# Optimization experiments

Measured on AMD Instinct MI355X. Metric: run time of the kernel, lower is better.

Reference implementation:

```python
import jax, jax.numpy as jnp
import numpy as np
from functools import partial

B, T, IN, H, NC, L = 2048, 512, 64, 64, 4, 2


def _lstm_layer(x, w_ih, w_hh, b_ih, b_hh):
    """Single PyTorch-convention LSTM layer. x: [B,T,Din]; gates ordered i,f,g,o.
    Returns full hidden sequence [B,T,H]."""
    Bx = x.shape[0]
    Hh = w_hh.shape[1]
    # precompute input contribution for all timesteps: [T,B,4H]
    xg = jnp.einsum('bti,gi->tbg', x, w_ih) + (b_ih + b_hh)

    def step(carry, xg_t):
        h, c = carry
        gates = xg_t + h @ w_hh.T  # [B,4H]
        i, f, g, o = jnp.split(gates, 4, axis=-1)
        i = jax.nn.sigmoid(i)
        f = jax.nn.sigmoid(f)
        g = jnp.tanh(g)
        o = jax.nn.sigmoid(o)
        c = f * c + i * g
        h = o * jnp.tanh(c)
        return (h, c), h

    h0 = jnp.zeros((Bx, Hh), dtype=x.dtype)
    c0 = jnp.zeros((Bx, Hh), dtype=x.dtype)
    (_, _), hs = jax.lax.scan(step, (h0, c0), xg)  # hs: [T,B,H]
    return jnp.swapaxes(hs, 0, 1)  # [B,T,H]


def setup_inputs() -> dict:
    key = jax.random.key(0)
    ks = jax.random.split(key, 16)
    s_in = 1.0 / np.sqrt(H)
    inp = {"x": jax.random.normal(ks[0], (B, T, IN), dtype=jnp.float32)}
    dims = [IN, H]
    for l in range(L):
        inp[f"w_ih{l}"] = jax.random.uniform(ks[1 + 4 * l], (4 * H, dims[l]), jnp.float32, -s_in, s_in)
        inp[f"w_hh{l}"] = jax.random.uniform(ks[2 + 4 * l], (4 * H, H), jnp.float32, -s_in, s_in)
        inp[f"b_ih{l}"] = jax.random.uniform(ks[3 + 4 * l], (4 * H,), jnp.float32, -s_in, s_in)
        inp[f"b_hh{l}"] = jax.random.uniform(ks[4 + 4 * l], (4 * H,), jnp.float32, -s_in, s_in)
    inp["fc_w"] = jax.random.uniform(ks[9], (NC, H), jnp.float32, -s_in, s_in)
    inp["fc_b"] = jax.random.uniform(ks[10], (NC,), jnp.float32, -s_in, s_in)
    return inp


def reference(x, w_ih0, w_hh0, b_ih0, b_hh0, w_ih1, w_hh1, b_ih1, b_hh1, fc_w, fc_b):
    # layer 0
    h1 = _lstm_layer(x, w_ih0, w_hh0, b_ih0, b_hh0)   # [B,T,H]
    # inter-layer dropout: identity at inference
    h2 = _lstm_layer(h1, w_ih1, w_hh1, b_ih1, b_hh1)  # [B,T,H]
    last = h2[:, -1, :]                                # [B,H]; dropout = identity (eval)
    return last @ fc_w.T + fc_b                        # [B,NC]
```

## Files before the change

### kernel.cpp

```cpp
#include <hip/hip_runtime.h>
#include <stdint.h>


#define T_SEQ 512
#define NB    4
#define PSTR  136

typedef __attribute__((ext_vector_type(8))) short  short8;
typedef __attribute__((ext_vector_type(4))) float  float4v;

__device__ __forceinline__ unsigned short f2bf(float f) {
    unsigned int u = __builtin_bit_cast(unsigned int, f);
    return (unsigned short)((u + 0x7FFFu + ((u >> 16) & 1u)) >> 16);
}
__device__ __forceinline__ float bf2f(unsigned short h) {
    unsigned int u = ((unsigned int)h) << 16;
    return __builtin_bit_cast(float, u);
}
__device__ __forceinline__ float sigm(float x) {
    return __builtin_amdgcn_rcpf(1.0f + __builtin_amdgcn_exp2f(-1.44269504088896f * x));
}
__device__ __forceinline__ float tanh_f(float x) {
    float a = __builtin_fabsf(x);
    float e = __builtin_amdgcn_exp2f(-2.88539008177793f * a);
    float t = (1.0f - e) * __builtin_amdgcn_rcpf(1.0f + e);
    return __builtin_copysignf(t, x);
}
__device__ __forceinline__ float permx32(float v) {
    int p = __builtin_amdgcn_ds_bpermute((int)((threadIdx.x & 63) ^ 32) << 2,
                                         __builtin_bit_cast(int, v));
    return __builtin_bit_cast(float, p);
}

__global__ __launch_bounds__(512, 4) void lstm2_kernel(
    const float* __restrict__ x,
    const float* __restrict__ wih0, const float* __restrict__ whh0,
    const float* __restrict__ bih0, const float* __restrict__ bhh0,
    const float* __restrict__ wih1, const float* __restrict__ whh1,
    const float* __restrict__ bih1, const float* __restrict__ bhh1,
    const float* __restrict__ fcw,  const float* __restrict__ fcb,
    float* __restrict__ out)
{
    __shared__ __align__(16) unsigned short panel0[2][16 * PSTR];
    __shared__ __align__(16) unsigned short panel1[2][16 * PSTR];
    __shared__ float h2buf[NB * 64];
    __shared__ float fcw_s[256];
    __shared__ float fcb_s[4];

    const int tid  = threadIdx.x;
    const int lane = tid & 63;
    const int wave = tid >> 6;
    const int mrow = lane & 15;
    const int kg   = lane >> 4;
    const int lset = wave >> 2;
    const int ws   = wave & 3;
    const int b0   = blockIdx.x * NB;

    for (int i = tid; i < 256; i += 512) fcw_s[i] = fcw[i];
    if (tid < 4) fcb_s[tid] = fcb[tid];
    for (int i = tid; i < 2 * 16 * PSTR; i += 512) {
        panel0[0][i] = 0; panel1[0][i] = 0;
    }

    const float* wih  = lset ? wih1 : wih0;
    const float* whh  = lset ? whh1 : whh0;
    const float* bihp = lset ? bih1 : bih0;
    const float* bhhp = lset ? bhh1 : bhh0;

    float biasg[4];
    #pragma unroll
    for (int g = 0; g < 4; ++g) {
        const int idx = g * 64 + ws * 16 + mrow;
        biasg[g] = bihp[idx] + bhhp[idx];
    }

    short8 whiF[4][4];
    #pragma unroll
    for (int g = 0; g < 4; ++g) {
        const int n = (g * 4 + ws) * 16 + mrow;
        #pragma unroll
        for (int kt = 0; kt < 4; ++kt) {
            const int k0 = kt * 32 + kg * 8;
            const float* src = (k0 < 64) ? (wih + n * 64 + k0)
                                         : (whh + n * 64 + (k0 - 64));
            union { short8 s; unsigned short u[8]; } hi8;
            #pragma unroll
            for (int j = 0; j < 8; ++j) hi8.u[j] = f2bf(src[j]);
            whiF[g][kt] = hi8.s;
        }
    }

    __syncthreads();
    if (tid < 256) {
        const int bx = tid >> 6, kx = tid & 63;
        const int xr = (bx & 1) + ((bx & 2) << 1);
        float xv = x[((size_t)(b0 + bx) * T_SEQ + 0) * 64 + kx];
        unsigned short h = f2bf(xv);
        panel0[0][xr * PSTR + kx]       = h;
        panel0[0][(xr + 8) * PSTR + kx] = f2bf(xv - bf2f(h));
    }
    __syncthreads();

    const int bcell = ((kg & 1) << 1) | (kg >> 1);
    const int hrow  = (bcell & 1) + ((bcell & 2) << 1);
    const int hcol  = ws * 16 + mrow;
    const int xrow  = (wave & 1) + ((wave & 2) << 1);
    float c = 0.f;

    for (int s = 0; s <= T_SEQ; ++s) {
        const int p = s & 1;
        const unsigned short* rd = lset ? panel1[p] : panel0[p];
        unsigned short* wr0 = panel0[p ^ 1];
        unsigned short* wr1 = panel1[p ^ 1];

        float xv = 0.f;
        if (lset == 0 && s < T_SEQ) {
            const int tn = (s + 1 < T_SEQ) ? (s + 1) : (T_SEQ - 1);
            xv = x[((size_t)(b0 + wave) * T_SEQ + tn) * 64 + lane];
        }

        short8 af[4];
        #pragma unroll
        for (int kt = 0; kt < 4; ++kt)
            af[kt] = *(const short8*)(rd + mrow * PSTR + kt * 32 + kg * 8);
        float4v acc[4];
        #pragma unroll
        for (int g = 0; g < 4; ++g) acc[g] = (float4v){0.f, 0.f, 0.f, 0.f};
        #pragma unroll
        for (int kt = 0; kt < 4; ++kt) {
            #pragma unroll
            for (int g = 0; g < 4; ++g)
                acc[g] = __builtin_amdgcn_mfma_f32_16x16x32_bf16(af[kt], whiF[g][kt], acc[g], 0, 0, 0);
        }

        const bool active = lset ? (s > 0) : (s < T_SEQ);
        if (active) {
            float gate[4];
            #pragma unroll
            for (int g = 0; g < 4; ++g) {
                float f0 = acc[g][0] + permx32(acc[g][0]);
                float f1 = acc[g][1] + permx32(acc[g][1]);
                gate[g] = ((kg & 2) ? f1 : f0) + biasg[g];
            }
            float ig = sigm(gate[0]), fg = sigm(gate[1]);
            float gt = tanh_f(gate[2]), og = sigm(gate[3]);
            c = fg * c + ig * gt;
            float hv = og * tanh_f(c);
            unsigned short hhi = f2bf(hv);
            unsigned short hlo = f2bf(hv - bf2f(hhi));
            if (lset == 0) {
                wr0[hrow * PSTR + 64 + hcol]       = hhi;
                wr0[(hrow + 8) * PSTR + 64 + hcol] = hlo;
                wr1[hrow * PSTR + hcol]            = hhi;
                wr1[(hrow + 8) * PSTR + hcol]      = hlo;
            } else {
                wr1[hrow * PSTR + 64 + hcol]       = hhi;
                wr1[(hrow + 8) * PSTR + 64 + hcol] = hlo;
                if (s == T_SEQ) h2buf[bcell * 64 + hcol] = hv;
            }
        }
        if (lset == 0 && s < T_SEQ) {
            unsigned short xh = f2bf(xv);
            wr0[xrow * PSTR + lane]       = xh;
            wr0[(xrow + 8) * PSTR + lane] = f2bf(xv - bf2f(xh));
        }
        __syncthreads();
    }

    if (tid < 16) {
        const int bb = tid >> 2, nc = tid & 3;
        float s = fcb_s[nc];
        #pragma unroll 8
        for (int h = 0; h < 64; ++h) s += h2buf[bb * 64 + h] * fcw_s[nc * 64 + h];
        out[(size_t)(b0 + bb) * 4 + nc] = s;
    }
}

extern "C" void kernel_launch(void* const* d_in, const int* in_sizes, int n_in,
                              void* d_out, int out_size, void* d_ws, size_t ws_size,
                              hipStream_t stream) {
    const float* x    = (const float*)d_in[0];
    const float* wih0 = (const float*)d_in[1];
    const float* whh0 = (const float*)d_in[2];
    const float* bih0 = (const float*)d_in[3];
    const float* bhh0 = (const float*)d_in[4];
    const float* wih1 = (const float*)d_in[5];
    const float* whh1 = (const float*)d_in[6];
    const float* bih1 = (const float*)d_in[7];
    const float* bhh1 = (const float*)d_in[8];
    const float* fcw  = (const float*)d_in[9];
    const float* fcb  = (const float*)d_in[10];
    float* out = (float*)d_out;
    (void)d_ws; (void)ws_size; (void)in_sizes; (void)n_in; (void)out_size;

    lstm2_kernel<<<dim3(2048 / NB), dim3(512), 0, stream>>>(
        x, wih0, whh0, bih0, bhh0, wih1, whh1, bih1, bhh1, fcw, fcb, out);
}
```

Measured before the change: 801.7 us.

## Relayout LSTM panels so MFMA rows pair hi/lo splits, removing cross-lane permutes

Reorganises the bf16 hi/lo split panel layout so each batch's hi and lo rows sit in adjacent MFMA rows. Gate sums then come from adding two accumulator elements in the same lane, which removes the ds_bpermute cross-lane reductions. Layer 0's h is written once and layer 1 reads it directly from panel0, so duplicate LDS writes are dropped. The x staging moves to the layer-1 waves, and the change also simplifies tanh, uses a cheaper round-half-up bf16 conversion, and zero-inits the first MFMA accumulator. The tanh formula without an absolute value may lose accuracy or overflow for large negative inputs.

Result: faster. 667.2 us (-16.8%).

```diff
diff --git a/kernel.cpp b/kernel.cpp
--- a/kernel.cpp
+++ b/kernel.cpp
@@ -5,6 +5,7 @@
 #define T_SEQ 512
 #define NB    4
 #define PSTR  136
+#define PANEL (16 * PSTR)
 
 typedef __attribute__((ext_vector_type(8))) short  short8;
 typedef __attribute__((ext_vector_type(4))) float  float4v;
@@ -12,6 +13,10 @@
 __device__ __forceinline__ unsigned short f2bf(float f) {
     unsigned int u = __builtin_bit_cast(unsigned int, f);
     return (unsigned short)((u + 0x7FFFu + ((u >> 16) & 1u)) >> 16);
+}
+__device__ __forceinline__ unsigned short f2bf_rhu(float f) {
+    unsigned int u = __builtin_bit_cast(unsigned int, f);
+    return (unsigned short)((u + 0x8000u) >> 16);
 }
 __device__ __forceinline__ float bf2f(unsigned short h) {
     unsigned int u = ((unsigned int)h) << 16;
@@ -21,15 +26,8 @@
     return __builtin_amdgcn_rcpf(1.0f + __builtin_amdgcn_exp2f(-1.44269504088896f * x));
 }
 __device__ __forceinline__ float tanh_f(float x) {
-    float a = __builtin_fabsf(x);
-    float e = __builtin_amdgcn_exp2f(-2.88539008177793f * a);
-    float t = (1.0f - e) * __builtin_amdgcn_rcpf(1.0f + e);
-    return __builtin_copysignf(t, x);
-}
-__device__ __forceinline__ float permx32(float v) {
-    int p = __builtin_amdgcn_ds_bpermute((int)((threadIdx.x & 63) ^ 32) << 2,
-                                         __builtin_bit_cast(int, v));
-    return __builtin_bit_cast(float, p);
+    float e = __builtin_amdgcn_exp2f(-2.88539008177793f * x);
+    return __builtin_fmaf(2.0f, __builtin_amdgcn_rcpf(1.0f + e), -1.0f);
 }
 
 __global__ __launch_bounds__(512, 4) void lstm2_kernel(
@@ -41,8 +39,8 @@
     const float* __restrict__ fcw,  const float* __restrict__ fcb,
     float* __restrict__ out)
 {
-    __shared__ __align__(16) unsigned short panel0[2][16 * PSTR];
-    __shared__ __align__(16) unsigned short panel1[2][16 * PSTR];
+    __shared__ __align__(16) unsigned short panel0[2][PANEL];
+    __shared__ __align__(16) unsigned short panel1[2][PANEL];
     __shared__ float h2buf[NB * 64];
     __shared__ float fcw_s[256];
     __shared__ float fcb_s[4];
@@ -58,7 +56,7 @@
 
     for (int i = tid; i < 256; i += 512) fcw_s[i] = fcw[i];
     if (tid < 4) fcb_s[tid] = fcb[tid];
-    for (int i = tid; i < 2 * 16 * PSTR; i += 512) {
+    for (int i = tid; i < 2 * PANEL; i += 512) {
         panel0[0][i] = 0; panel1[0][i] = 0;
     }
 
@@ -93,41 +91,50 @@
     __syncthreads();
     if (tid < 256) {
         const int bx = tid >> 6, kx = tid & 63;
-        const int xr = (bx & 1) + ((bx & 2) << 1);
         float xv = x[((size_t)(b0 + bx) * T_SEQ + 0) * 64 + kx];
-        unsigned short h = f2bf(xv);
-        panel0[0][xr * PSTR + kx]       = h;
-        panel0[0][(xr + 8) * PSTR + kx] = f2bf(xv - bf2f(h));
+        unsigned short h = f2bf_rhu(xv);
+        panel0[0][(4 * bx) * PSTR + kx]     = h;
+        panel0[0][(4 * bx + 1) * PSTR + kx] = f2bf_rhu(xv - bf2f(h));
     }
     __syncthreads();
 
-    const int bcell = ((kg & 1) << 1) | (kg >> 1);
-    const int hrow  = (bcell & 1) + ((bcell & 2) << 1);
+    const int fragoff = mrow * PSTR + kg * 8;
+    const unsigned short* rdA = &panel0[0][0] + (lset ? 64 : 0) + fragoff;
+    const unsigned short* rdB = (lset ? &panel1[0][0] : &panel0[0][0]) + fragoff;
+    unsigned short* hP = lset ? &panel1[0][0] : &panel0[0][0];
     const int hcol  = ws * 16 + mrow;
-    const int xrow  = (wave & 1) + ((wave & 2) << 1);
+    const int hoff0 = (4 * kg) * PSTR + 64 + hcol;
+    const int hoff1 = hoff0 + PSTR;
+    const int bw    = wave & 3;
+    const int xr0   = (4 * bw) * PSTR + lane;
+    const float* xp = x + ((size_t)(b0 + bw) * T_SEQ + 1) * 64 + lane;
     float c = 0.f;
+    const float4v z4 = {0.f, 0.f, 0.f, 0.f};
 
     for (int s = 0; s <= T_SEQ; ++s) {
-        const int p = s & 1;
-        const unsigned short* rd = lset ? panel1[p] : panel0[p];
-        unsigned short* wr0 = panel0[p ^ 1];
-        unsigned short* wr1 = panel1[p ^ 1];
+        const int p    = s & 1;
+        const int poff = p * PANEL;
+        const int qoff = poff ^ PANEL;
 
+        const bool do_stage = (lset == 1) && (s + 1 < T_SEQ);
         float xv = 0.f;
-        if (lset == 0 && s < T_SEQ) {
-            const int tn = (s + 1 < T_SEQ) ? (s + 1) : (T_SEQ - 1);
-            xv = x[((size_t)(b0 + wave) * T_SEQ + tn) * 64 + lane];
-        }
+        if (do_stage) xv = *xp;
 
         short8 af[4];
-        #pragma unroll
-        for (int kt = 0; kt < 4; ++kt)
-            af[kt] = *(const short8*)(rd + mrow * PSTR + kt * 32 + kg * 8);
+        {
+            const unsigned short* bA = rdA + poff;
+            const unsigned short* bB = rdB + poff;
+            af[0] = *(const short8*)(bA);
+            af[1] = *(const short8*)(bA + 32);
+            af[2] = *(const short8*)(bB + 64);
+            af[3] = *(const short8*)(bB + 96);
+        }
         float4v acc[4];
         #pragma unroll
-        for (int g = 0; g < 4; ++g) acc[g] = (float4v){0.f, 0.f, 0.f, 0.f};
+        for (int g = 0; g < 4; ++g)
+            acc[g] = __builtin_amdgcn_mfma_f32_16x16x32_bf16(af[0], whiF[g][0], z4, 0, 0, 0);
         #pragma unroll
-        for (int kt = 0; kt < 4; ++kt) {
+        for (int kt = 1; kt < 4; ++kt) {
             #pragma unroll
             for (int g = 0; g < 4; ++g)
                 acc[g] = __builtin_amdgcn_mfma_f32_16x16x32_bf16(af[kt], whiF[g][kt], acc[g], 0, 0, 0);
@@ -135,34 +142,28 @@
 
         const bool active = lset ? (s > 0) : (s < T_SEQ);
         if (active) {
-            float gate[4];
-            #pragma unroll
-            for (int g = 0; g < 4; ++g) {
-                float f0 = acc[g][0] + permx32(acc[g][0]);
-                float f1 = acc[g][1] + permx32(acc[g][1]);
-                gate[g] = ((kg & 2) ? f1 : f0) + biasg[g];
-            }
-            float ig = sigm(gate[0]), fg = sigm(gate[1]);
-            float gt = tanh_f(gate[2]), og = sigm(gate[3]);
+            float g0 = acc[0][0] + acc[0][1] + biasg[0];
+            float g1 = acc[1][0] + acc[1][1] + biasg[1];
+            float g2 = acc[2][0] + acc[2][1] + biasg[2];
+            float g3 = acc[3][0] + acc[3][1] + biasg[3];
+            float ig = sigm(g0), fg = sigm(g1);
+            float gt = tanh_f(g2), og = sigm(g3);
             c = fg * c + ig * gt;
             float hv = og * tanh_f(c);
-            unsigned short hhi = f2bf(hv);
-            unsigned short hlo = f2bf(hv - bf2f(hhi));
-            if (lset == 0) {
-                wr0[hrow * PSTR + 64 + hcol]       = hhi;
-                wr0[(hrow + 8) * PSTR + 64 + hcol] = hlo;
-                wr1[hrow * PSTR + hcol]            = hhi;
-                wr1[(hrow + 8) * PSTR + hcol]      = hlo;
-            } else {
-                wr1[hrow * PSTR + 64 + hcol]       = hhi;
-                wr1[(hrow + 8) * PSTR + 64 + hcol] = hlo;
-                if (s == T_SEQ) h2buf[bcell * 64 + hcol] = hv;
-            }
+            unsigned short hhi = f2bf_rhu(hv);
+            unsigned short hlo = f2bf_rhu(hv - bf2f(hhi));
+            unsigned short* w = hP + qoff;
+            w[hoff0] = hhi;
+            w[hoff1] = hlo;
+            if (lset && s == T_SEQ) h2buf[(kg << 6) + hcol] = hv;
         }
-        if (lset == 0 && s < T_SEQ) {
-            unsigned short xh = f2bf(xv);
-            wr0[xrow * PSTR + lane]       = xh;
-            wr0[(xrow + 8) * PSTR + lane] = f2bf(xv - bf2f(xh));
+        if (do_stage) {
+            unsigned short xh = f2bf_rhu(xv);
+            unsigned short xl = f2bf_rhu(xv - bf2f(xh));
+            unsigned short* w0 = &panel0[0][0] + qoff + xr0;
+            w0[0]    = xh;
+            w0[PSTR] = xl;
+            xp += 64;
         }
         __syncthreads();
     }
```
